# Kernel optimization log

Hardware: AMD Instinct MI355X
Metric: run time of the kernel (lower is better)

Reference implementation:

```python
import jax, jax.numpy as jnp
import numpy as np

COL = 14
NJ = 14
SIGMA = 1.0
RADIUS = int(4.0 * SIGMA + 0.5)  # scipy gaussian_filter default truncate=4.0 -> radius 4

def _gaussian_matrix():
    # 1D operator matrix G[y_out, y_src] of scipy.ndimage.gaussian_filter with
    # sigma=1, mode='reflect' (== numpy 'symmetric' padding) on a length-COL axis.
    w = np.exp(-0.5 * (np.arange(-RADIUS, RADIUS + 1) / SIGMA) ** 2)
    w = w / w.sum()
    eye_p = np.pad(np.eye(COL), ((RADIUS, RADIUS), (0, 0)), mode='symmetric')
    G = sum(w[k] * eye_p[k:k + COL] for k in range(2 * RADIUS + 1))
    return jnp.asarray(G.astype(np.float32))

G_MAT = _gaussian_matrix()

def setup_inputs():
    key = jax.random.key(0)
    k1, k2, k3 = jax.random.split(key, 3)
    B = 8192
    out = jax.random.normal(k1, (B, 3 * NJ, COL, COL), dtype=jnp.float32)
    t = jax.random.uniform(k2, (B, NJ, 2), dtype=jnp.float32)  # normalized coords in [0,1)
    v = jax.random.randint(k3, (B, NJ, 1), 0, 2).astype(jnp.float32)
    v = jnp.tile(v, (1, 1, 2))  # visibility flag duplicated over (x,y) channels
    return {"out": out, "t": t, "v": v}

def _forward(out, t, v):
    B = out.shape[0]
    scale = 1.0 / COL
    h = out[:, :NJ]          # [B,NJ,COL,COL] heatmaps
    o = out[:, NJ:]          # [B,2*NJ,COL,COL] offset maps (x offsets then y offsets)
    # per-joint argmax over flattened grid (first-occurrence, same as torch .max)
    idx = jnp.argmax(h.reshape(B, NJ, COL * COL), axis=-1)    # [B,NJ]
    yc = idx // COL
    xc = idx % COL
    # gather offsets at the argmax location
    o_flat = o.reshape(B, 2 * NJ, COL * COL)
    ox = jnp.take_along_axis(o_flat[:, :NJ], idx[:, :, None], axis=2)[..., 0]
    oy = jnp.take_along_axis(o_flat[:, NJ:], idx[:, :, None], axis=2)[..., 0]
    x_pred = jnp.stack([(ox + xc.astype(out.dtype)) * scale,
                        (oy + yc.astype(out.dtype)) * scale], axis=-1)  # [B,NJ,2]
    # gaussian target construction (constant w.r.t. the network output)
    ti = (t * COL).astype(jnp.int32)      # int() truncation; t >= 0
    xi, yi = ti[..., 0], ti[..., 1]
    inb = (xi >= 0) & (xi <= COL - 1) & (yi >= 0) & (yi <= COL - 1)
    vis = v[..., 0].astype(jnp.int32) == 1
    scat = vis & inb                       # joints that receive a gaussian target
    v_eff = jnp.where((vis & ~inb)[..., None], 0.0, v)  # out-of-bounds visible -> zeroed
    # gaussian-filtered one-hot == outer(G[:,yi], G[:,xi]) (separable splat)
    gy = G_MAT.T[jnp.clip(yi, 0, COL - 1)]   # [B,NJ,COL]
    gx = G_MAT.T[jnp.clip(xi, 0, COL - 1)]   # [B,NJ,COL]
    tt = gy[..., :, None] * gx[..., None, :]  # [B,NJ,COL,COL]
    mn = tt.min(axis=(2, 3), keepdims=True)
    mx = tt.max(axis=(2, 3), keepdims=True)
    tt = jnp.where(scat[..., None, None], (tt - mn) / (mx - mn), 0.0)
    # heatmap loss; original zeroes only ROW 0 of the map for invisible joints
    diff1 = h - tt
    vis_eff = (v_eff[..., 0].astype(jnp.int32) == 1)
    diff1 = diff1.at[:, :, 0, :].set(diff1[:, :, 0, :] * vis_eff[..., None].astype(diff1.dtype))
    cnt = jnp.sum(vis_eff.astype(jnp.float32))
    d1 = jnp.sum(diff1 * diff1) / cnt
    # coordinate loss, masked by (possibly updated) visibility
    diff2 = (x_pred - t) * v_eff
    n2 = v_eff.sum() / 2.0
    d2 = jnp.sum(diff2 * diff2) / n2
    return d1 + d2

def reference(out, t, v):
    return _forward(out, t, v)
```

## Files before the change

kernel.cpp:

```cpp
#include <hip/hip_runtime.h>


#define COL 14
#define NJ 14
#define CELLS (COL * COL)
#define THREADS 256
#define WPB (THREADS / 64)
#define BLOCKS 2048
#define NSLOT 16

__global__ __launch_bounds__(THREADS)
void mse3_main(const float* __restrict__ outp, const float* __restrict__ tp,
               const float* __restrict__ vp, double* __restrict__ acc, int npair)
{
    __shared__ float Gs[CELLS];
    __shared__ float cminS[COL], cmaxS[COL];
    __shared__ double part[WPB][4];

    const int tid = threadIdx.x;

    if (tid < CELLS) {
        const double wraw[9] = {3.3546262790251185e-4, 1.1108996538242306e-2,
                                1.353352832366127e-1,  6.065306597126334e-1, 1.0,
                                6.065306597126334e-1,  1.353352832366127e-1,
                                1.1108996538242306e-2, 3.3546262790251185e-4};
        const double Z = 2.5066208042307818;
        int gi = tid / COL;
        int gj = tid - COL * gi;
        double a = 0.0;
#pragma unroll
        for (int k = 0; k < 9; ++k) {
            int r = gi + k;
            int m = (r < 4) ? (3 - r) : ((r < 18) ? (r - 4) : (31 - r));
            if (m == gj) a += wraw[k] / Z;
        }
        Gs[tid] = (float)a;
    }
    __syncthreads();
    if (tid < COL) {
        float mn = Gs[tid], mx = mn;
        for (int r = 1; r < COL; ++r) {
            float g = Gs[r * COL + tid];
            mn = fminf(mn, g);
            mx = fmaxf(mx, g);
        }
        cminS[tid] = mn;
        cmaxS[tid] = mx;
    }
    __syncthreads();

    const int lane  = tid & 63;
    const int gwave = blockIdx.x * WPB + (tid >> 6);
    const int nwaves = BLOCKS * WPB;

    float s1 = 0.0f;
    float s2 = 0.0f, cnt = 0.0f, n2 = 0.0f;

    for (int p = gwave; p < npair; p += nwaves) {
        const int b = p / NJ;
        const int j = p - NJ * b;
        const float* hptr = outp + ((size_t)b * (3 * NJ) + j) * CELLS;

        float4 hv = make_float4(0.f, 0.f, 0.f, 0.f);
        float best = -3.402823466e38f;
        int bidx = 0;
        if (lane < 49) {
            hv = reinterpret_cast<const float4*>(hptr)[lane];
            best = hv.x; bidx = 4 * lane;
            if (hv.y > best) { best = hv.y; bidx = 4 * lane + 1; }
            if (hv.z > best) { best = hv.z; bidx = 4 * lane + 2; }
            if (hv.w > best) { best = hv.w; bidx = 4 * lane + 3; }
        }
#pragma unroll
        for (int off = 32; off >= 1; off >>= 1) {
            float ov = __shfl_down(best, off, 64);
            int   oi = __shfl_down(bidx, off, 64);
            if (ov > best || (ov == best && oi < bidx)) { best = ov; bidx = oi; }
        }
        const int idx = __shfl(bidx, 0, 64);

        int pack = 0;
        if (lane == 0) {
            float ox = hptr[NJ * CELLS + idx];
            float oy = hptr[2 * NJ * CELLS + idx];
            float2 tv = reinterpret_cast<const float2*>(tp)[p];
            float2 vv = reinterpret_cast<const float2*>(vp)[p];
            int xi = (int)(tv.x * 14.0f);
            int yi = (int)(tv.y * 14.0f);
            bool inb  = (xi >= 0) && (xi <= COL - 1) && (yi >= 0) && (yi <= COL - 1);
            bool vis  = ((int)vv.x == 1);
            bool scat = vis && inb;
            float ve0 = (vis && !inb) ? 0.0f : vv.x;
            float ve1 = (vis && !inb) ? 0.0f : vv.y;
            bool vise = ((int)ve0 == 1);
            int yc = idx / COL;
            int xc = idx - COL * yc;
            const float SCALE = (float)(1.0 / 14.0);
            float dx = (ox + (float)xc) * SCALE - tv.x;
            float dy = (oy + (float)yc) * SCALE - tv.y;
            dx *= ve0;
            dy *= ve1;
            s2 += dx * dx + dy * dy;
            if (vise) cnt += 1.0f;
            n2 += ve0 + ve1;
            int xic = min(max(xi, 0), COL - 1);
            int yic = min(max(yi, 0), COL - 1);
            pack = xic | (yic << 4) | (scat ? 256 : 0) | (vise ? 512 : 0);
        }
        pack = __shfl(pack, 0, 64);
        const int  xic  = pack & 15;
        const int  yic  = (pack >> 4) & 15;
        const bool scat = (pack & 256) != 0;
        const bool vise = (pack & 512) != 0;

        if (lane < 49) {
            float h4[4] = {hv.x, hv.y, hv.z, hv.w};
            int e0 = 4 * lane;
            int y = e0 / COL;
            int x = e0 - COL * y;
            if (scat) {
                float mn  = cminS[yic] * cminS[xic];
                float mx  = cmaxS[yic] * cmaxS[xic];
                float inv = 1.0f / (mx - mn);
#pragma unroll
                for (int c = 0; c < 4; ++c) {
                    float tt = (Gs[y * COL + yic] * Gs[x * COL + xic] - mn) * inv;
                    float d = h4[c] - tt;
                    if (y == 0 && !vise) d = 0.0f;
                    s1 += d * d;
                    ++x; if (x == COL) { x = 0; ++y; }
                }
            } else {
#pragma unroll
                for (int c = 0; c < 4; ++c) {
                    float d = h4[c];
                    if (y == 0 && !vise) d = 0.0f;
                    s1 += d * d;
                    ++x; if (x == COL) { x = 0; ++y; }
                }
            }
        }
    }

#pragma unroll
    for (int off = 32; off >= 1; off >>= 1) s1 += __shfl_down(s1, off, 64);

    const int w = tid >> 6;
    if (lane == 0) {
        part[w][0] = (double)s1;
        part[w][1] = (double)s2;
        part[w][2] = (double)cnt;
        part[w][3] = (double)n2;
    }
    __syncthreads();
    if (tid == 0) {
        double a0 = 0, a1 = 0, a2 = 0, a3 = 0;
        for (int i = 0; i < WPB; ++i) {
            a0 += part[i][0]; a1 += part[i][1];
            a2 += part[i][2]; a3 += part[i][3];
        }
        double* slot = acc + (size_t)(blockIdx.x & (NSLOT - 1)) * 4;
        unsafeAtomicAdd(&slot[0], a0);
        unsafeAtomicAdd(&slot[1], a1);
        unsafeAtomicAdd(&slot[2], a2);
        unsafeAtomicAdd(&slot[3], a3);
    }
}

__global__ void mse3_final(const double* __restrict__ acc, float* __restrict__ o)
{
    double s1 = 0, s2 = 0, cnt = 0, n2 = 0;
    for (int i = 0; i < NSLOT; ++i) {
        s1  += acc[i * 4 + 0];
        s2  += acc[i * 4 + 1];
        cnt += acc[i * 4 + 2];
        n2  += acc[i * 4 + 3];
    }
    o[0] = (float)(s1 / cnt + s2 / (0.5 * n2));
}

extern "C" void kernel_launch(void* const* d_in, const int* in_sizes, int n_in,
                              void* d_out, int out_size, void* d_ws, size_t ws_size,
                              hipStream_t stream)
{
    const float* outp = (const float*)d_in[0];
    const float* tp   = (const float*)d_in[1];
    const float* vp   = (const float*)d_in[2];
    double* acc = (double*)d_ws;

    const int B = in_sizes[0] / (3 * NJ * CELLS);
    const int npair = B * NJ;

    hipMemsetAsync(d_ws, 0, NSLOT * 4 * sizeof(double), stream);
    mse3_main<<<BLOCKS, THREADS, 0, stream>>>(outp, tp, vp, acc, npair);
    mse3_final<<<1, 1, 0, stream>>>(acc, (float*)d_out);
}
```

Baseline: 350.5 us.

## Batch per-wave joint metadata, prefetch next heatmap, replace atomics with partials

Each wave now handles up to 16 joint pairs per batch. One lane per pair loads its target and visibility up front and broadcasts the packed flags. The next heatmap float4 is prefetched while the current one is reduced. The offset gathers and the coordinate loss move to a per-lane pass after the loop. Global double atomics and the memset are replaced by per-block partial writes plus a 256-thread final reduction, which removes atomic contention and one launch, at the cost of more registers and an extra dependency on the index buffer.

```diff
diff --git a/kernel.cpp b/kernel.cpp
--- a/kernel.cpp
+++ b/kernel.cpp
@@ -7,11 +7,12 @@
 #define THREADS 256
 #define WPB (THREADS / 64)
 #define BLOCKS 2048
-#define NSLOT 16
+#define MAXI 16
+#define NEGINF -3.402823466e38f
 
 __global__ __launch_bounds__(THREADS)
 void mse3_main(const float* __restrict__ outp, const float* __restrict__ tp,
-               const float* __restrict__ vp, double* __restrict__ acc, int npair)
+               const float* __restrict__ vp, double* __restrict__ partial, int npair)
 {
     __shared__ float Gs[CELLS];
     __shared__ float cminS[COL], cmaxS[COL];
@@ -49,108 +50,137 @@
     }
     __syncthreads();
 
-    const int lane  = tid & 63;
-    const int gwave = blockIdx.x * WPB + (tid >> 6);
+    const int lane   = tid & 63;
+    const int wv     = tid >> 6;
+    const int gwave  = blockIdx.x * WPB + wv;
     const int nwaves = BLOCKS * WPB;
 
-    float s1 = 0.0f;
-    float s2 = 0.0f, cnt = 0.0f, n2 = 0.0f;
-
-    for (int p = gwave; p < npair; p += nwaves) {
-        const int b = p / NJ;
-        const int j = p - NJ * b;
-        const float* hptr = outp + ((size_t)b * (3 * NJ) + j) * CELLS;
-
-        float4 hv = make_float4(0.f, 0.f, 0.f, 0.f);
-        float best = -3.402823466e38f;
-        int bidx = 0;
-        if (lane < 49) {
-            hv = reinterpret_cast<const float4*>(hptr)[lane];
-            best = hv.x; bidx = 4 * lane;
-            if (hv.y > best) { best = hv.y; bidx = 4 * lane + 1; }
-            if (hv.z > best) { best = hv.z; bidx = 4 * lane + 2; }
-            if (hv.w > best) { best = hv.w; bidx = 4 * lane + 3; }
-        }
-#pragma unroll
-        for (int off = 32; off >= 1; off >>= 1) {
-            float ov = __shfl_down(best, off, 64);
-            int   oi = __shfl_down(bidx, off, 64);
-            if (ov > best || (ov == best && oi < bidx)) { best = ov; bidx = oi; }
-        }
-        const int idx = __shfl(bidx, 0, 64);
-
-        int pack = 0;
-        if (lane == 0) {
-            float ox = hptr[NJ * CELLS + idx];
-            float oy = hptr[2 * NJ * CELLS + idx];
+    float s1 = 0.0f, s2 = 0.0f, cnt = 0.0f, n2 = 0.0f;
+
+    for (int pbase = gwave; pbase < npair; pbase += nwaves * MAXI) {
+        const int m = min(MAXI, (npair - pbase + nwaves - 1) / nwaves);
+
+        int packreg = 0;
+        float tvx = 0.f, tvy = 0.f, vvx = 0.f, vvy = 0.f;
+        if (lane < m) {
+            int p = pbase + lane * nwaves;
             float2 tv = reinterpret_cast<const float2*>(tp)[p];
             float2 vv = reinterpret_cast<const float2*>(vp)[p];
+            tvx = tv.x; tvy = tv.y; vvx = vv.x; vvy = vv.y;
             int xi = (int)(tv.x * 14.0f);
             int yi = (int)(tv.y * 14.0f);
-            bool inb  = (xi >= 0) && (xi <= COL - 1) && (yi >= 0) && (yi <= COL - 1);
-            bool vis  = ((int)vv.x == 1);
-            bool scat = vis && inb;
-            float ve0 = (vis && !inb) ? 0.0f : vv.x;
-            float ve1 = (vis && !inb) ? 0.0f : vv.y;
-            bool vise = ((int)ve0 == 1);
-            int yc = idx / COL;
-            int xc = idx - COL * yc;
-            const float SCALE = (float)(1.0 / 14.0);
-            float dx = (ox + (float)xc) * SCALE - tv.x;
-            float dy = (oy + (float)yc) * SCALE - tv.y;
-            dx *= ve0;
-            dy *= ve1;
+            bool inb    = (xi >= 0) && (xi <= COL - 1) && (yi >= 0) && (yi <= COL - 1);
+            bool vis    = ((int)vv.x == 1);
+            bool scat   = vis && inb;
+            bool zeroed = vis && !inb;
+            float ve0   = zeroed ? 0.0f : vv.x;
+            bool vise   = ((int)ve0 == 1);
+            int xic = min(max(xi, 0), COL - 1);
+            int yic = min(max(yi, 0), COL - 1);
+            packreg = xic | (yic << 4) | (scat ? 256 : 0) | (vise ? 512 : 0)
+                          | (zeroed ? 1024 : 0);
+        }
+
+        float4 hv_next = make_float4(0.f, 0.f, 0.f, 0.f);
+        if (lane < 49) {
+            int b = pbase / NJ, j = pbase - NJ * b;
+            hv_next = reinterpret_cast<const float4*>(
+                outp + ((size_t)b * (3 * NJ) + j) * CELLS)[lane];
+        }
+
+        int myidx = 0;
+        for (int i = 0; i < m; ++i) {
+            float4 hv = hv_next;
+            if (i + 1 < m && lane < 49) {
+                int p = pbase + (i + 1) * nwaves;
+                int b = p / NJ, j = p - NJ * b;
+                hv_next = reinterpret_cast<const float4*>(
+                    outp + ((size_t)b * (3 * NJ) + j) * CELLS)[lane];
+            }
+            const int pk = __shfl(packreg, i, 64);
+            const int xic = pk & 15;
+            const int yic = (pk >> 4) & 15;
+            const bool scat = (pk & 256) != 0;
+            const bool vise = (pk & 512) != 0;
+
+            float best = NEGINF;
+            int bidx = 0;
+            if (lane < 49) {
+                best = hv.x; bidx = 4 * lane;
+                if (hv.y > best) { best = hv.y; bidx = 4 * lane + 1; }
+                if (hv.z > best) { best = hv.z; bidx = 4 * lane + 2; }
+                if (hv.w > best) { best = hv.w; bidx = 4 * lane + 3; }
+            }
+#pragma unroll
+            for (int off = 32; off >= 1; off >>= 1) {
+                float ov = __shfl_down(best, off, 64);
+                int   oi = __shfl_down(bidx, off, 64);
+                if (ov > best || (ov == best && oi < bidx)) { best = ov; bidx = oi; }
+            }
+            const int idxb = __shfl(bidx, 0, 64);
+            if (lane == i) myidx = idxb;
+
+            if (lane < 49) {
+                float h4[4] = {hv.x, hv.y, hv.z, hv.w};
+                int y = (4 * lane) / COL;
+                int x = 4 * lane - COL * y;
+                if (scat) {
+                    float mn  = cminS[yic] * cminS[xic];
+                    float mx  = cmaxS[yic] * cmaxS[xic];
+                    float inv = 1.0f / (mx - mn);
+#pragma unroll
+                    for (int c = 0; c < 4; ++c) {
+                        float tt = (Gs[y * COL + yic] * Gs[x * COL + xic] - mn) * inv;
+                        float d = h4[c] - tt;
+                        if (y == 0 && !vise) d = 0.0f;
+                        s1 += d * d;
+                        ++x; if (x == COL) { x = 0; ++y; }
+                    }
+                } else {
+#pragma unroll
+                    for (int c = 0; c < 4; ++c) {
+                        float d = h4[c];
+                        if (y == 0 && !vise) d = 0.0f;
+                        s1 += d * d;
+                        ++x; if (x == COL) { x = 0; ++y; }
+                    }
+                }
+            }
+        }
+
+        if (lane < m) {
+            int p = pbase + lane * nwaves;
+            int b = p / NJ, j = p - NJ * b;
+            const float* base = outp + (size_t)b * (3 * NJ) * CELLS;
+            float ox = base[(size_t)(NJ + j) * CELLS + myidx];
+            float oy = base[(size_t)(2 * NJ + j) * CELLS + myidx];
+            bool zeroed = (packreg & 1024) != 0;
+            bool vise   = (packreg & 512) != 0;
+            float ve0 = zeroed ? 0.0f : vvx;
+            float ve1 = zeroed ? 0.0f : vvy;
+            int yc = myidx / COL;
+            int xc = myidx - COL * yc;
+            const float SC = (float)(1.0 / 14.0);
+            float dx = (ox + (float)xc) * SC - tvx; dx *= ve0;
+            float dy = (oy + (float)yc) * SC - tvy; dy *= ve1;
             s2 += dx * dx + dy * dy;
             if (vise) cnt += 1.0f;
             n2 += ve0 + ve1;
-            int xic = min(max(xi, 0), COL - 1);
-            int yic = min(max(yi, 0), COL - 1);
-            pack = xic | (yic << 4) | (scat ? 256 : 0) | (vise ? 512 : 0);
-        }
-        pack = __shfl(pack, 0, 64);
-        const int  xic  = pack & 15;
-        const int  yic  = (pack >> 4) & 15;
-        const bool scat = (pack & 256) != 0;
-        const bool vise = (pack & 512) != 0;
-
-        if (lane < 49) {
-            float h4[4] = {hv.x, hv.y, hv.z, hv.w};
-            int e0 = 4 * lane;
-            int y = e0 / COL;
-            int x = e0 - COL * y;
-            if (scat) {
-                float mn  = cminS[yic] * cminS[xic];
-                float mx  = cmaxS[yic] * cmaxS[xic];
-                float inv = 1.0f / (mx - mn);
-#pragma unroll
-                for (int c = 0; c < 4; ++c) {
-                    float tt = (Gs[y * COL + yic] * Gs[x * COL + xic] - mn) * inv;
-                    float d = h4[c] - tt;
-                    if (y == 0 && !vise) d = 0.0f;
-                    s1 += d * d;
-                    ++x; if (x == COL) { x = 0; ++y; }
-                }
-            } else {
-#pragma unroll
-                for (int c = 0; c < 4; ++c) {
-                    float d = h4[c];
-                    if (y == 0 && !vise) d = 0.0f;
-                    s1 += d * d;
-                    ++x; if (x == COL) { x = 0; ++y; }
-                }
-            }
-        }
-    }
-
-#pragma unroll
-    for (int off = 32; off >= 1; off >>= 1) s1 += __shfl_down(s1, off, 64);
-
-    const int w = tid >> 6;
+        }
+    }
+
+#pragma unroll
+    for (int off = 32; off >= 1; off >>= 1) {
+        s1  += __shfl_down(s1,  off, 64);
+        s2  += __shfl_down(s2,  off, 64);
+        cnt += __shfl_down(cnt, off, 64);
+        n2  += __shfl_down(n2,  off, 64);
+    }
     if (lane == 0) {
-        part[w][0] = (double)s1;
-        part[w][1] = (double)s2;
-        part[w][2] = (double)cnt;
-        part[w][3] = (double)n2;
+        part[wv][0] = (double)s1;
+        part[wv][1] = (double)s2;
+        part[wv][2] = (double)cnt;
+        part[wv][3] = (double)n2;
     }
     __syncthreads();
     if (tid == 0) {
@@ -159,24 +189,37 @@
             a0 += part[i][0]; a1 += part[i][1];
             a2 += part[i][2]; a3 += part[i][3];
         }
-        double* slot = acc + (size_t)(blockIdx.x & (NSLOT - 1)) * 4;
-        unsafeAtomicAdd(&slot[0], a0);
-        unsafeAtomicAdd(&slot[1], a1);
-        unsafeAtomicAdd(&slot[2], a2);
-        unsafeAtomicAdd(&slot[3], a3);
+        double* o = partial + (size_t)blockIdx.x * 4;
+        o[0] = a0; o[1] = a1; o[2] = a2; o[3] = a3;
     }
 }
 
-__global__ void mse3_final(const double* __restrict__ acc, float* __restrict__ o)
+__global__ __launch_bounds__(256)
+void mse3_final(const double* __restrict__ partial, float* __restrict__ o)
 {
-    double s1 = 0, s2 = 0, cnt = 0, n2 = 0;
-    for (int i = 0; i < NSLOT; ++i) {
-        s1  += acc[i * 4 + 0];
-        s2  += acc[i * 4 + 1];
-        cnt += acc[i * 4 + 2];
-        n2  += acc[i * 4 + 3];
-    }
-    o[0] = (float)(s1 / cnt + s2 / (0.5 * n2));
+    __shared__ double p2[4][4];
+    double a0 = 0, a1 = 0, a2 = 0, a3 = 0;
+    for (int b = threadIdx.x; b < BLOCKS; b += 256) {
+        const double* q = partial + (size_t)b * 4;
+        a0 += q[0]; a1 += q[1]; a2 += q[2]; a3 += q[3];
+    }
+#pragma unroll
+    for (int off = 32; off >= 1; off >>= 1) {
+        a0 += __shfl_down(a0, off, 64);
+        a1 += __shfl_down(a1, off, 64);
+        a2 += __shfl_down(a2, off, 64);
+        a3 += __shfl_down(a3, off, 64);
+    }
+    const int lane = threadIdx.x & 63, wv = threadIdx.x >> 6;
+    if (lane == 0) { p2[wv][0] = a0; p2[wv][1] = a1; p2[wv][2] = a2; p2[wv][3] = a3; }
+    __syncthreads();
+    if (threadIdx.x == 0) {
+        double s1 = 0, s2 = 0, cn = 0, nn = 0;
+        for (int i = 0; i < 4; ++i) {
+            s1 += p2[i][0]; s2 += p2[i][1]; cn += p2[i][2]; nn += p2[i][3];
+        }
+        o[0] = (float)(s1 / cn + s2 / (0.5 * nn));
+    }
 }
 
 extern "C" void kernel_launch(void* const* d_in, const int* in_sizes, int n_in,
@@ -186,12 +229,11 @@
     const float* outp = (const float*)d_in[0];
     const float* tp   = (const float*)d_in[1];
     const float* vp   = (const float*)d_in[2];
-    double* acc = (double*)d_ws;
+    double* partial = (double*)d_ws;
 
     const int B = in_sizes[0] / (3 * NJ * CELLS);
     const int npair = B * NJ;
 
-    hipMemsetAsync(d_ws, 0, NSLOT * 4 * sizeof(double), stream);
-    mse3_main<<<BLOCKS, THREADS, 0, stream>>>(outp, tp, vp, acc, npair);
-    mse3_final<<<1, 1, 0, stream>>>(acc, (float*)d_out);
+    mse3_main<<<BLOCKS, THREADS, 0, stream>>>(outp, tp, vp, partial, npair);
+    mse3_final<<<1, 256, 0, stream>>>(partial, (float*)d_out);
 }
```

Result: faster. 331.8 us (-5.3%).
